# Kernel optimization log

Hardware: AMD Instinct MI355X
Metric: run time of the kernel (lower is better)

## Reference

```python
import jax, jax.numpy as jnp
import numpy as np

H = 100  # hidden size of both LSTM layers (fixed in the module)

def lstm_layer(x, w_ih, w_hh, b_ih, b_hh):
    # x: [B, T, I]; w_ih: [4H, I]; w_hh: [4H, H]; biases: [4H]
    # PyTorch gate order: input, forget, cell(g), output.
    B, T, _ = x.shape
    xg = jnp.einsum('bti,gi->btg', x, w_ih) + b_ih + b_hh  # [B, T, 4H], input GEMM hoisted out of the scan
    h0 = jnp.zeros((B, H), x.dtype)
    c0 = jnp.zeros((B, H), x.dtype)
    w_hh_t = w_hh.T  # [H, 4H]

    def step(carry, xg_t):
        h, c = carry
        g = xg_t + h @ w_hh_t                # [B, 4H]
        i, f, gg, o = jnp.split(g, 4, axis=-1)
        i = jax.nn.sigmoid(i)
        f = jax.nn.sigmoid(f)
        gg = jnp.tanh(gg)
        o = jax.nn.sigmoid(o)
        c = f * c + i * gg
        h = o * jnp.tanh(c)
        return (h, c), h

    _, hs = jax.lax.scan(step, (h0, c0), jnp.swapaxes(xg, 0, 1))  # hs: [T, B, H]
    return jnp.swapaxes(hs, 0, 1)  # [B, T, H]


def setup_inputs() -> dict:
    key = jax.random.key(0)
    ks = jax.random.split(key, 13)
    B, T, I = 256, 2048, 8
    s = lambda fan: 1.0 / np.sqrt(fan)
    u = lambda k, shape, fan: jax.random.uniform(k, shape, jnp.float32, -s(fan), s(fan))
    return {
        'x': jax.random.normal(ks[0], (B, T, I), jnp.float32),
        'w_ih1': u(ks[1], (4 * H, I), H), 'w_hh1': u(ks[2], (4 * H, H), H),
        'b_ih1': u(ks[3], (4 * H,), H), 'b_hh1': u(ks[4], (4 * H,), H),
        'w_ih2': u(ks[5], (4 * H, H), H), 'w_hh2': u(ks[6], (4 * H, H), H),
        'b_ih2': u(ks[7], (4 * H,), H), 'b_hh2': u(ks[8], (4 * H,), H),
        'fc1_w': u(ks[9], (25, H), H), 'fc1_b': u(ks[10], (25,), H),
        'fc2_w': u(ks[11], (1, 25), 25), 'fc2_b': u(ks[12], (1,), 25),
    }


def reference(x, w_ih1, w_hh1, b_ih1, b_hh1, w_ih2, w_hh2, b_ih2, b_hh2,
              fc1_w, fc1_b, fc2_w, fc2_b):
    # Dropout layers are identity in eval mode.
    h1 = lstm_layer(x, w_ih1, w_hh1, b_ih1, b_hh1)    # [B, T, H]
    h2 = lstm_layer(h1, w_ih2, w_hh2, b_ih2, b_hh2)   # [B, T, H]
    last = h2[:, -1, :]                               # [B, H]
    y = last @ fc1_w.T + fc1_b                        # [B, 25]
    return y @ fc2_w.T + fc2_b                        # [B, 1]
```

## Files before the change

### kernel.cpp

```cpp
#include <hip/hip_runtime.h>

#define BB 256
#define TT 2048
#define HD 100

typedef _Float16 h2v __attribute__((ext_vector_type(2)));

__device__ __forceinline__ float fdot2(unsigned w, unsigned h, float c) {
#if __has_builtin(__builtin_amdgcn_fdot2)
    return __builtin_amdgcn_fdot2(__builtin_bit_cast(h2v, w),
                                  __builtin_bit_cast(h2v, h), c, false);
#else
    h2v a = __builtin_bit_cast(h2v, w), b = __builtin_bit_cast(h2v, h);
    c = fmaf((float)a[0], (float)b[0], c);
    c = fmaf((float)a[1], (float)b[1], c);
    return c;
#endif
}
__device__ __forceinline__ unsigned packh2(float a, float b) {
    h2v p; p[0] = (_Float16)a; p[1] = (_Float16)b;
    return __builtin_bit_cast(unsigned, p);
}
__device__ __forceinline__ float rcp_f(float x) {
#if __has_builtin(__builtin_amdgcn_rcpf)
    return __builtin_amdgcn_rcpf(x);
#else
    return 1.0f / x;
#endif
}
__device__ __forceinline__ float act_f(float x, float m, float s, float d) {
    return fmaf(m, rcp_f(1.0f + __expf(-s * x)), d);
}
__device__ __forceinline__ float tanh_f(float x) {
    return fmaf(2.0f, rcp_f(1.0f + __expf(-2.0f * x)), -1.0f);
}

__global__ __launch_bounds__(512, 1) void lstm_fused(
    const float* __restrict__ x,
    const float* __restrict__ w_ih1, const float* __restrict__ w_hh1,
    const float* __restrict__ b_ih1, const float* __restrict__ b_hh1,
    const float* __restrict__ w_ih2, const float* __restrict__ w_hh2,
    const float* __restrict__ b_ih2, const float* __restrict__ b_hh2,
    const float* __restrict__ fc1_w, const float* __restrict__ fc1_b,
    const float* __restrict__ fc2_w, const float* __restrict__ fc2_b,
    float* __restrict__ out)
{
    const int b    = blockIdx.x;
    const int tid  = threadIdx.x;
    const int lane = tid & 63;
    const int grp  = tid >> 8;
    const int lt   = tid & 255;

    __shared__ unsigned h1p[64];
    __shared__ unsigned h2p[64];
    __shared__ __align__(16) unsigned xs[2][32][4];
    __shared__ float g1[400];
    __shared__ float g2[400];
    __shared__ float h2f[HD];
    __shared__ float fca[25];

    const bool isG = lt < 200;
    const int  gt  = isG ? lt : 199;
    const int  um  = lt >> 2;
    const bool isU = ((lt & 3) == 3) && isG;
    const bool isX = (grp == 0) && (lt >= 200) && (lt < 232);
    const int  xsl = lt - 200;

    unsigned wreg[200];
    float bias0, bias1, cc0 = 0.f, cc1 = 0.f;

    const int g0 = 2 * gt, g1r = 2 * gt + 1;
    if (grp == 0) {
        { const float4* p = (const float4*)(w_ih1 + (size_t)g0 * 8);
          float4 v0 = p[0], v1 = p[1];
          wreg[0] = packh2(v0.x, v0.y); wreg[1] = packh2(v0.z, v0.w);
          wreg[2] = packh2(v1.x, v1.y); wreg[3] = packh2(v1.z, v1.w); }
        { const float4* p = (const float4*)(w_ih1 + (size_t)g1r * 8);
          float4 v0 = p[0], v1 = p[1];
          wreg[54] = packh2(v0.x, v0.y); wreg[55] = packh2(v0.z, v0.w);
          wreg[56] = packh2(v1.x, v1.y); wreg[57] = packh2(v1.z, v1.w); }
        { const float4* p = (const float4*)(w_hh1 + (size_t)g0 * HD);
          #pragma unroll
          for (int q = 0; q < 25; ++q) {
              float4 v = p[q];
              wreg[4 + 2*q] = packh2(v.x, v.y); wreg[5 + 2*q] = packh2(v.z, v.w);
          } }
        { const float4* p = (const float4*)(w_hh1 + (size_t)g1r * HD);
          #pragma unroll
          for (int q = 0; q < 25; ++q) {
              float4 v = p[q];
              wreg[58 + 2*q] = packh2(v.x, v.y); wreg[59 + 2*q] = packh2(v.z, v.w);
          } }
        bias0 = b_ih1[g0] + b_hh1[g0];
        bias1 = b_ih1[g1r] + b_hh1[g1r];
    } else {
        { const float4* p = (const float4*)(w_ih2 + (size_t)g0 * HD);
          #pragma unroll
          for (int q = 0; q < 25; ++q) {
              float4 v = p[q];
              wreg[2*q] = packh2(v.x, v.y); wreg[2*q + 1] = packh2(v.z, v.w);
          } }
        { const float4* p = (const float4*)(w_ih2 + (size_t)g1r * HD);
          #pragma unroll
          for (int q = 0; q < 25; ++q) {
              float4 v = p[q];
              wreg[50 + 2*q] = packh2(v.x, v.y); wreg[51 + 2*q] = packh2(v.z, v.w);
          } }
        { const float4* p = (const float4*)(w_hh2 + (size_t)g0 * HD);
          #pragma unroll
          for (int q = 0; q < 25; ++q) {
              float4 v = p[q];
              wreg[100 + 2*q] = packh2(v.x, v.y); wreg[101 + 2*q] = packh2(v.z, v.w);
          } }
        { const float4* p = (const float4*)(w_hh2 + (size_t)g1r * HD);
          #pragma unroll
          for (int q = 0; q < 25; ++q) {
              float4 v = p[q];
              wreg[150 + 2*q] = packh2(v.x, v.y); wreg[151 + 2*q] = packh2(v.z, v.w);
          } }
        bias0 = b_ih2[g0] + b_hh2[g0];
        bias1 = b_ih2[g1r] + b_hh2[g1r];
    }
    const bool tg = (gt >= 100) && (gt < 150);
    const float am = tg ? 2.0f : 1.0f;
    const float as = tg ? 2.0f : 1.0f;
    const float ad = tg ? -1.0f : 0.0f;

    if (tid < 64) { h1p[tid] = 0u; h2p[tid] = 0u; }
    if (isX) {
        const float4* p = (const float4*)(x + ((size_t)b * TT + xsl) * 8);
        float4 v0 = p[0], v1 = p[1];
        xs[0][xsl][0] = packh2(v0.x, v0.y); xs[0][xsl][1] = packh2(v0.z, v0.w);
        xs[0][xsl][2] = packh2(v1.x, v1.y); xs[0][xsl][3] = packh2(v1.z, v1.w);
    }
    __syncthreads();

    float4 pa = {0,0,0,0}, pb = {0,0,0,0};

    #pragma unroll 1
    for (int i = 0; i <= TT; ++i) {
        const bool pf = ((i & 31) == 0) && (i + 32 < TT);
        if (grp == 0) {
            if (i < TT) {
                if (isX && pf) {
                    const float4* p = (const float4*)(x + ((size_t)b * TT + i + 32 + xsl) * 8);
                    pa = p[0]; pb = p[1];
                }
                const unsigned st = h1p[lane];
                const unsigned* xq = xs[(i >> 5) & 1][i & 31];
                unsigned x0 = xq[0], x1 = xq[1], x2 = xq[2], x3 = xq[3];
                float a0 = bias0, a1 = bias1, a2 = 0.f, a3 = 0.f;
                a0 = fdot2(wreg[0], x0, a0); a2 = fdot2(wreg[1], x1, a2);
                a0 = fdot2(wreg[2], x2, a0); a2 = fdot2(wreg[3], x3, a2);
                a1 = fdot2(wreg[54], x0, a1); a3 = fdot2(wreg[55], x1, a3);
                a1 = fdot2(wreg[56], x2, a1); a3 = fdot2(wreg[57], x3, a3);
                #pragma unroll
                for (int k = 0; k < 50; ++k) {
                    unsigned hk = (unsigned)__builtin_amdgcn_readlane((int)st, k);
                    if (k & 1) { a2 = fdot2(wreg[4 + k], hk, a2); a3 = fdot2(wreg[58 + k], hk, a3); }
                    else       { a0 = fdot2(wreg[4 + k], hk, a0); a1 = fdot2(wreg[58 + k], hk, a1); }
                }
                float r0 = act_f(a0 + a2, am, as, ad);
                float r1 = act_f(a1 + a3, am, as, ad);
                if (isG) *(float2*)(g1 + 2 * gt) = make_float2(r0, r1);
            }
        } else {
            if (i >= 1) {
                const unsigned cur = h1p[lane];
                const unsigned st2 = h2p[lane];
                float a0 = bias0, a1 = bias1, a2 = 0.f, a3 = 0.f;
                #pragma unroll
                for (int k = 0; k < 50; ++k) {
                    unsigned hk = (unsigned)__builtin_amdgcn_readlane((int)cur, k);
                    if (k & 1) { a2 = fdot2(wreg[k], hk, a2); a3 = fdot2(wreg[50 + k], hk, a3); }
                    else       { a0 = fdot2(wreg[k], hk, a0); a1 = fdot2(wreg[50 + k], hk, a1); }
                }
                #pragma unroll
                for (int k = 0; k < 50; ++k) {
                    unsigned hk = (unsigned)__builtin_amdgcn_readlane((int)st2, k);
                    if (k & 1) { a2 = fdot2(wreg[100 + k], hk, a2); a3 = fdot2(wreg[150 + k], hk, a3); }
                    else       { a0 = fdot2(wreg[100 + k], hk, a0); a1 = fdot2(wreg[150 + k], hk, a1); }
                }
                float r0 = act_f(a0 + a2, am, as, ad);
                float r1 = act_f(a1 + a3, am, as, ad);
                if (isG) *(float2*)(g2 + 2 * gt) = make_float2(r0, r1);
            }
        }
        __syncthreads();
        if (grp == 0) {
            if (i < TT) {
                if (isU) {
                    const int j = 2 * um;
                    float2 gi = *(const float2*)(g1 + j);
                    float2 gf = *(const float2*)(g1 + 100 + j);
                    float2 gg = *(const float2*)(g1 + 200 + j);
                    float2 go = *(const float2*)(g1 + 300 + j);
                    cc0 = gf.x * cc0 + gi.x * gg.x;
                    cc1 = gf.y * cc1 + gi.y * gg.y;
                    float h0 = go.x * tanh_f(cc0);
                    float h1v = go.y * tanh_f(cc1);
                    h1p[um] = packh2(h0, h1v);
                }
                if (isX && pf) {
                    const int nb2 = ((i >> 5) + 1) & 1;
                    xs[nb2][xsl][0] = packh2(pa.x, pa.y); xs[nb2][xsl][1] = packh2(pa.z, pa.w);
                    xs[nb2][xsl][2] = packh2(pb.x, pb.y); xs[nb2][xsl][3] = packh2(pb.z, pb.w);
                }
            }
        } else {
            if (i >= 1 && isU) {
                const int j = 2 * um;
                float2 gi = *(const float2*)(g2 + j);
                float2 gf = *(const float2*)(g2 + 100 + j);
                float2 gg = *(const float2*)(g2 + 200 + j);
                float2 go = *(const float2*)(g2 + 300 + j);
                cc0 = gf.x * cc0 + gi.x * gg.x;
                cc1 = gf.y * cc1 + gi.y * gg.y;
                float h0 = go.x * tanh_f(cc0);
                float h1v = go.y * tanh_f(cc1);
                h2p[um] = packh2(h0, h1v);
                if (i == TT) { h2f[j] = h0; h2f[j + 1] = h1v; }
            }
        }
        __syncthreads();
    }

    if (tid < 25) {
        float a = fc1_b[tid];
        const float* wp = fc1_w + tid * HD;
        #pragma unroll
        for (int k = 0; k < HD; ++k) a += h2f[k] * wp[k];
        fca[tid] = a;
    }
    __syncthreads();
    if (tid == 0) {
        float y = fc2_b[0];
        #pragma unroll
        for (int m = 0; m < 25; ++m) y += fca[m] * fc2_w[m];
        out[b] = y;
    }
}

extern "C" void kernel_launch(void* const* d_in, const int* in_sizes, int n_in,
                              void* d_out, int out_size, void* d_ws, size_t ws_size,
                              hipStream_t stream) {
    const float* x     = (const float*)d_in[0];
    const float* w_ih1 = (const float*)d_in[1];
    const float* w_hh1 = (const float*)d_in[2];
    const float* b_ih1 = (const float*)d_in[3];
    const float* b_hh1 = (const float*)d_in[4];
    const float* w_ih2 = (const float*)d_in[5];
    const float* w_hh2 = (const float*)d_in[6];
    const float* b_ih2 = (const float*)d_in[7];
    const float* b_hh2 = (const float*)d_in[8];
    const float* fc1_w = (const float*)d_in[9];
    const float* fc1_b = (const float*)d_in[10];
    const float* fc2_w = (const float*)d_in[11];
    const float* fc2_b = (const float*)d_in[12];
    float* out = (float*)d_out;

    lstm_fused<<<BB, 512, 0, stream>>>(x, w_ih1, w_hh1, b_ih1, b_hh1,
                                       w_ih2, w_hh2, b_ih2, b_hh2,
                                       fc1_w, fc1_b, fc2_w, fc2_b, out);
}
```

Before: 2.771 ms.

## Split layer-2 input and recurrent matvecs across separate thread groups

Moves from 512 to 768 threads per block, so layer 2's input-projection and recurrent matvecs run on two separate 256-thread groups that write partial sums to shared memory. Layer 1 moves to a third group. The cell update for layer 2 now adds the partials and applies the activations inside 50 dedicated update threads, and the update threads move from every fourth lane to a contiguous range. This halves the per-thread serial dot-product chain on the critical path and cuts register use from 200 to 108 packed weights. In exchange it adds more waves to synchronise and puts the activation work on the update path.

```diff
diff --git a/kernel.cpp b/kernel.cpp
--- a/kernel.cpp
+++ b/kernel.cpp
@@ -28,14 +28,15 @@
     return 1.0f / x;
 #endif
 }
+__device__ __forceinline__ float sigmoid_f(float x) { return rcp_f(1.0f + __expf(-x)); }
+__device__ __forceinline__ float tanh_f(float x) {
+    return fmaf(2.0f, rcp_f(1.0f + __expf(-2.0f * x)), -1.0f);
+}
 __device__ __forceinline__ float act_f(float x, float m, float s, float d) {
     return fmaf(m, rcp_f(1.0f + __expf(-s * x)), d);
 }
-__device__ __forceinline__ float tanh_f(float x) {
-    return fmaf(2.0f, rcp_f(1.0f + __expf(-2.0f * x)), -1.0f);
-}
-
-__global__ __launch_bounds__(512, 1) void lstm_fused(
+
+__global__ __launch_bounds__(768, 1) void lstm_fused(
     const float* __restrict__ x,
     const float* __restrict__ w_ih1, const float* __restrict__ w_hh1,
     const float* __restrict__ b_ih1, const float* __restrict__ b_hh1,
@@ -54,23 +55,53 @@
     __shared__ unsigned h1p[64];
     __shared__ unsigned h2p[64];
     __shared__ __align__(16) unsigned xs[2][32][4];
+    __shared__ float pI[400];
+    __shared__ float pH[400];
     __shared__ float g1[400];
-    __shared__ float g2[400];
     __shared__ float h2f[HD];
     __shared__ float fca[25];
 
-    const bool isG = lt < 200;
-    const int  gt  = isG ? lt : 199;
-    const int  um  = lt >> 2;
-    const bool isU = ((lt & 3) == 3) && isG;
-    const bool isX = (grp == 0) && (lt >= 200) && (lt < 232);
+    const bool isGate = lt < 200;
+    const int  gt  = isGate ? lt : 199;
+    const bool isU = (lt >= 200) && (lt < 250);
+    const int  u   = lt - 200;
+    const bool isX = (grp == 2) && (lt >= 200) && (lt < 232);
     const int  xsl = lt - 200;
 
-    unsigned wreg[200];
-    float bias0, bias1, cc0 = 0.f, cc1 = 0.f;
+    unsigned wreg[108];
+    float bias0 = 0.f, bias1 = 0.f;
+    float cc0 = 0.f, cc1 = 0.f;
 
     const int g0 = 2 * gt, g1r = 2 * gt + 1;
     if (grp == 0) {
+        { const float4* p = (const float4*)(w_ih2 + (size_t)g0 * HD);
+          #pragma unroll
+          for (int q = 0; q < 25; ++q) {
+              float4 v = p[q];
+              wreg[2*q] = packh2(v.x, v.y); wreg[2*q+1] = packh2(v.z, v.w);
+          } }
+        { const float4* p = (const float4*)(w_ih2 + (size_t)g1r * HD);
+          #pragma unroll
+          for (int q = 0; q < 25; ++q) {
+              float4 v = p[q];
+              wreg[50 + 2*q] = packh2(v.x, v.y); wreg[51 + 2*q] = packh2(v.z, v.w);
+          } }
+        bias0 = b_ih2[g0] + b_hh2[g0];
+        bias1 = b_ih2[g1r] + b_hh2[g1r];
+    } else if (grp == 1) {
+        { const float4* p = (const float4*)(w_hh2 + (size_t)g0 * HD);
+          #pragma unroll
+          for (int q = 0; q < 25; ++q) {
+              float4 v = p[q];
+              wreg[2*q] = packh2(v.x, v.y); wreg[2*q+1] = packh2(v.z, v.w);
+          } }
+        { const float4* p = (const float4*)(w_hh2 + (size_t)g1r * HD);
+          #pragma unroll
+          for (int q = 0; q < 25; ++q) {
+              float4 v = p[q];
+              wreg[50 + 2*q] = packh2(v.x, v.y); wreg[51 + 2*q] = packh2(v.z, v.w);
+          } }
+    } else {
         { const float4* p = (const float4*)(w_ih1 + (size_t)g0 * 8);
           float4 v0 = p[0], v1 = p[1];
           wreg[0] = packh2(v0.x, v0.y); wreg[1] = packh2(v0.z, v0.w);
@@ -93,33 +124,6 @@
           } }
         bias0 = b_ih1[g0] + b_hh1[g0];
         bias1 = b_ih1[g1r] + b_hh1[g1r];
-    } else {
-        { const float4* p = (const float4*)(w_ih2 + (size_t)g0 * HD);
-          #pragma unroll
-          for (int q = 0; q < 25; ++q) {
-              float4 v = p[q];
-              wreg[2*q] = packh2(v.x, v.y); wreg[2*q + 1] = packh2(v.z, v.w);
-          } }
-        { const float4* p = (const float4*)(w_ih2 + (size_t)g1r * HD);
-          #pragma unroll
-          for (int q = 0; q < 25; ++q) {
-              float4 v = p[q];
-              wreg[50 + 2*q] = packh2(v.x, v.y); wreg[51 + 2*q] = packh2(v.z, v.w);
-          } }
-        { const float4* p = (const float4*)(w_hh2 + (size_t)g0 * HD);
-          #pragma unroll
-          for (int q = 0; q < 25; ++q) {
-              float4 v = p[q];
-              wreg[100 + 2*q] = packh2(v.x, v.y); wreg[101 + 2*q] = packh2(v.z, v.w);
-          } }
-        { const float4* p = (const float4*)(w_hh2 + (size_t)g1r * HD);
-          #pragma unroll
-          for (int q = 0; q < 25; ++q) {
-              float4 v = p[q];
-              wreg[150 + 2*q] = packh2(v.x, v.y); wreg[151 + 2*q] = packh2(v.z, v.w);
-          } }
-        bias0 = b_ih2[g0] + b_hh2[g0];
-        bias1 = b_ih2[g1r] + b_hh2[g1r];
     }
     const bool tg = (gt >= 100) && (gt < 150);
     const float am = tg ? 2.0f : 1.0f;
@@ -140,13 +144,13 @@
     #pragma unroll 1
     for (int i = 0; i <= TT; ++i) {
         const bool pf = ((i & 31) == 0) && (i + 32 < TT);
-        if (grp == 0) {
+        const unsigned st = (grp == 1) ? h2p[lane] : h1p[lane];
+        if (grp == 2) {
             if (i < TT) {
                 if (isX && pf) {
                     const float4* p = (const float4*)(x + ((size_t)b * TT + i + 32 + xsl) * 8);
                     pa = p[0]; pb = p[1];
                 }
-                const unsigned st = h1p[lane];
                 const unsigned* xq = xs[(i >> 5) & 1][i & 31];
                 unsigned x0 = xq[0], x1 = xq[1], x2 = xq[2], x3 = xq[3];
                 float a0 = bias0, a1 = bias1, a2 = 0.f, a3 = 0.f;
@@ -162,64 +166,60 @@
                 }
                 float r0 = act_f(a0 + a2, am, as, ad);
                 float r1 = act_f(a1 + a3, am, as, ad);
-                if (isG) *(float2*)(g1 + 2 * gt) = make_float2(r0, r1);
+                if (isGate) *(float2*)(g1 + 2 * gt) = make_float2(r0, r1);
             }
         } else {
             if (i >= 1) {
-                const unsigned cur = h1p[lane];
-                const unsigned st2 = h2p[lane];
                 float a0 = bias0, a1 = bias1, a2 = 0.f, a3 = 0.f;
                 #pragma unroll
                 for (int k = 0; k < 50; ++k) {
-                    unsigned hk = (unsigned)__builtin_amdgcn_readlane((int)cur, k);
+                    unsigned hk = (unsigned)__builtin_amdgcn_readlane((int)st, k);
                     if (k & 1) { a2 = fdot2(wreg[k], hk, a2); a3 = fdot2(wreg[50 + k], hk, a3); }
                     else       { a0 = fdot2(wreg[k], hk, a0); a1 = fdot2(wreg[50 + k], hk, a1); }
                 }
-                #pragma unroll
-                for (int k = 0; k < 50; ++k) {
-                    unsigned hk = (unsigned)__builtin_amdgcn_readlane((int)st2, k);
-                    if (k & 1) { a2 = fdot2(wreg[100 + k], hk, a2); a3 = fdot2(wreg[150 + k], hk, a3); }
-                    else       { a0 = fdot2(wreg[100 + k], hk, a0); a1 = fdot2(wreg[150 + k], hk, a1); }
-                }
-                float r0 = act_f(a0 + a2, am, as, ad);
-                float r1 = act_f(a1 + a3, am, as, ad);
-                if (isG) *(float2*)(g2 + 2 * gt) = make_float2(r0, r1);
+                float* dst = (grp == 0) ? pI : pH;
+                if (isGate) *(float2*)(dst + 2 * gt) = make_float2(a0 + a2, a1 + a3);
             }
         }
         __syncthreads();
         if (grp == 0) {
-            if (i < TT) {
-                if (isU) {
-                    const int j = 2 * um;
-                    float2 gi = *(const float2*)(g1 + j);
-                    float2 gf = *(const float2*)(g1 + 100 + j);
-                    float2 gg = *(const float2*)(g1 + 200 + j);
-                    float2 go = *(const float2*)(g1 + 300 + j);
-                    cc0 = gf.x * cc0 + gi.x * gg.x;
-                    cc1 = gf.y * cc1 + gi.y * gg.y;
-                    float h0 = go.x * tanh_f(cc0);
-                    float h1v = go.y * tanh_f(cc1);
-                    h1p[um] = packh2(h0, h1v);
-                }
-                if (isX && pf) {
-                    const int nb2 = ((i >> 5) + 1) & 1;
-                    xs[nb2][xsl][0] = packh2(pa.x, pa.y); xs[nb2][xsl][1] = packh2(pa.z, pa.w);
-                    xs[nb2][xsl][2] = packh2(pb.x, pb.y); xs[nb2][xsl][3] = packh2(pb.z, pb.w);
-                }
-            }
-        } else {
-            if (i >= 1 && isU) {
-                const int j = 2 * um;
-                float2 gi = *(const float2*)(g2 + j);
-                float2 gf = *(const float2*)(g2 + 100 + j);
-                float2 gg = *(const float2*)(g2 + 200 + j);
-                float2 go = *(const float2*)(g2 + 300 + j);
+            if (i < TT && isU) {
+                const int j = 2 * u;
+                float2 gi = *(const float2*)(g1 + j);
+                float2 gf = *(const float2*)(g1 + 100 + j);
+                float2 gg = *(const float2*)(g1 + 200 + j);
+                float2 go = *(const float2*)(g1 + 300 + j);
                 cc0 = gf.x * cc0 + gi.x * gg.x;
                 cc1 = gf.y * cc1 + gi.y * gg.y;
-                float h0 = go.x * tanh_f(cc0);
-                float h1v = go.y * tanh_f(cc1);
-                h2p[um] = packh2(h0, h1v);
+                h1p[u] = packh2(go.x * tanh_f(cc0), go.y * tanh_f(cc1));
+            }
+        } else if (grp == 1) {
+            if (i >= 1 && isU) {
+                const int j = 2 * u;
+                float2 sIi = *(const float2*)(pI + j);
+                float2 sHi = *(const float2*)(pH + j);
+                float2 sIf = *(const float2*)(pI + 100 + j);
+                float2 sHf = *(const float2*)(pH + 100 + j);
+                float2 sIg = *(const float2*)(pI + 200 + j);
+                float2 sHg = *(const float2*)(pH + 200 + j);
+                float2 sIo = *(const float2*)(pI + 300 + j);
+                float2 sHo = *(const float2*)(pH + 300 + j);
+                float gi0 = sigmoid_f(sIi.x + sHi.x), gi1 = sigmoid_f(sIi.y + sHi.y);
+                float gf0 = sigmoid_f(sIf.x + sHf.x), gf1 = sigmoid_f(sIf.y + sHf.y);
+                float gg0 = tanh_f(sIg.x + sHg.x),    gg1 = tanh_f(sIg.y + sHg.y);
+                float go0 = sigmoid_f(sIo.x + sHo.x), go1 = sigmoid_f(sIo.y + sHo.y);
+                cc0 = gf0 * cc0 + gi0 * gg0;
+                cc1 = gf1 * cc1 + gi1 * gg1;
+                float h0 = go0 * tanh_f(cc0);
+                float h1v = go1 * tanh_f(cc1);
+                h2p[u] = packh2(h0, h1v);
                 if (i == TT) { h2f[j] = h0; h2f[j + 1] = h1v; }
+            }
+        } else {
+            if (isX && pf) {
+                const int nb2 = ((i >> 5) + 1) & 1;
+                xs[nb2][xsl][0] = packh2(pa.x, pa.y); xs[nb2][xsl][1] = packh2(pa.z, pa.w);
+                xs[nb2][xsl][2] = packh2(pb.x, pb.y); xs[nb2][xsl][3] = packh2(pb.z, pb.w);
             }
         }
         __syncthreads();
@@ -259,7 +259,7 @@
     const float* fc2_b = (const float*)d_in[12];
     float* out = (float*)d_out;
 
-    lstm_fused<<<BB, 512, 0, stream>>>(x, w_ih1, w_hh1, b_ih1, b_hh1,
+    lstm_fused<<<BB, 768, 0, stream>>>(x, w_ih1, w_hh1, b_ih1, b_hh1,
                                        w_ih2, w_hh2, b_ih2, b_hh2,
                                        fc1_w, fc1_b, fc2_w, fc2_b, out);
 }
```

Measured after the change: 2.752 ms. Within noise of the previous version (-0.7%).
